# Performance work log

Hardware: AMD Instinct MI355X
Metric: run time of the kernel (lower is better)

Reference implementation:

```python
import jax, jax.numpy as jnp
import numpy as np


def setup_inputs() -> dict:
    key = jax.random.key(0)
    ks = jax.random.split(key, 4)
    B, N, D, C = 8, 32768, 128, 64
    H = D // 2
    features = jax.random.normal(ks[0], (B, N, D), dtype=jnp.float32)
    cluster_assignments = jax.random.randint(ks[1], (B, N), 0, C)
    W1 = jax.random.normal(ks[2], (D, H), dtype=jnp.float32) * (1.0 / np.sqrt(D))
    b1 = jnp.zeros((H,), dtype=jnp.float32)
    W2 = jax.random.normal(ks[3], (H, 1), dtype=jnp.float32) * (1.0 / np.sqrt(H))
    b2 = jnp.zeros((1,), dtype=jnp.float32)
    return {"features": features, "cluster_assignments": cluster_assignments,
            "W1": W1, "b1": b1, "W2": W2, "b2": b2, "num_clusters": C}


def reference(features, cluster_assignments, W1, b1, W2, b2, num_clusters):
    # features: [B, N, D]; cluster_assignments: [B, N] ints in [0, num_clusters)
    B, N, D = features.shape
    # importance_net: Linear -> ReLU -> Linear -> Sigmoid
    h = jax.nn.relu(jnp.einsum('bnd,dh->bnh', features, W1) + b1)
    imp = jax.nn.sigmoid(jnp.einsum('bnh,ho->bno', h, W2) + b2)[..., 0]  # [B, N]

    # Fused per-(batch, cluster) softmax-weighted segment sum.
    num_seg = B * num_clusters
    seg = (cluster_assignments + num_clusters * jnp.arange(B)[:, None]).reshape(-1)  # [B*N]
    imp_f = imp.reshape(-1)
    # stable softmax within each segment
    seg_max = jax.ops.segment_max(imp_f, seg, num_segments=num_seg)  # -inf for empty
    e = jnp.exp(imp_f - seg_max[seg])
    denom = jax.ops.segment_sum(e, seg, num_segments=num_seg)
    w = e / denom[seg]  # [B*N]
    out = jax.ops.segment_sum(features.reshape(-1, D) * w[:, None], seg,
                              num_segments=num_seg)  # empty clusters -> zeros
    return out.reshape(B, num_clusters, D)
```

## Files before the change

kernel.cpp:

```cpp
#include <hip/hip_runtime.h>
#include <hip/hip_bf16.h>


#define B_ 8
#define N_ 32768
#define D_ 128
#define C_ 64
#define H_ 64

#define NTHREADS 512
#define NWAVES 8
#define ROWS_PER_BLOCK 512
#define NBLOCKS ((B_ * N_) / ROWS_PER_BLOCK)
#define SLICES (NBLOCKS / B_)
#define NSS 4
#define RST 152
#define W1S 136

typedef float f32x4 __attribute__((ext_vector_type(4)));
typedef short s16x8 __attribute__((ext_vector_type(8)));

__device__ __forceinline__ short bf16rne(float x) {
    unsigned u = __float_as_uint(x);
    u = (u + 0x7FFFu + ((u >> 16) & 1u)) >> 16;
    return (short)u;
}
__device__ __forceinline__ float ubf_lo(unsigned u) {
    return __uint_as_float(u << 16);
}
__device__ __forceinline__ float ubf_hi(unsigned u) {
    return __uint_as_float(u & 0xFFFF0000u);
}

__device__ __forceinline__ s16x8 pk8(float4 a, float4 b) {
    union { s16x8 v; __hip_bfloat162 h[4]; } u;
    u.h[0] = __float22bfloat162_rn(make_float2(a.x, a.y));
    u.h[1] = __float22bfloat162_rn(make_float2(a.z, a.w));
    u.h[2] = __float22bfloat162_rn(make_float2(b.x, b.y));
    u.h[3] = __float22bfloat162_rn(make_float2(b.z, b.w));
    return u.v;
}

template <bool USE_WS>
__global__ __launch_bounds__(NTHREADS, 2)
void ca_fused_kernel(const float* __restrict__ features,
                     const int* __restrict__ ca,
                     const float* __restrict__ b1,
                     const float* __restrict__ W2,
                     const float* __restrict__ b2,
                     const float* __restrict__ W1,
                     float* __restrict__ out_sums,
                     float* __restrict__ denoms,
                     float* __restrict__ pout,
                     float* __restrict__ pden)
{
    __shared__ __align__(16) unsigned short ft[D_ * RST];
    __shared__ __align__(16) unsigned short w1l[H_ * W1S];
    __shared__ __align__(16) unsigned int ceu[128];

    const int tid  = threadIdx.x;
    const int lane = tid & 63;
    const int wave = tid >> 6;
    const int m    = lane & 15;
    const int kb   = lane >> 4;
    const int kbase = kb * 8;
    const int bidx = blockIdx.x;
    const int b    = bidx / SLICES;
    const int row_blk0 = bidx * ROWS_PER_BLOCK;

    for (int i = tid; i < H_ * D_; i += NTHREADS) {
        const int k = i >> 6, h = i & 63;
        w1l[h * W1S + k] = (unsigned short)bf16rne(W1[i]);
    }

    f32x4 w2v[4];
    unsigned b1p[8];
#pragma unroll
    for (int c4 = 0; c4 < 4; ++c4) {
#pragma unroll
        for (int qq = 0; qq < 4; ++qq)
            w2v[c4][qq] = W2[c4 * 16 + kb * 4 + qq];
#pragma unroll
        for (int hh = 0; hh < 2; ++hh) {
            const int i0 = c4 * 16 + kb * 4 + hh * 2;
            b1p[c4 * 2 + hh] =
                ((unsigned)(unsigned short)bf16rne(b1[i0 + 1]) << 16) |
                (unsigned)(unsigned short)bf16rne(b1[i0]);
        }
    }
    const float b2v = b2[0];

    const int CH = wave >> 1;
    const int dh = wave & 1;

    f32x4 accS[4];
    f32x4 accD = (f32x4){0.f, 0.f, 0.f, 0.f};
#pragma unroll
    for (int nt = 0; nt < 4; ++nt) accS[nt] = (f32x4){0.f, 0.f, 0.f, 0.f};

    s16x8 bones;
    {
        const short o = (m == 0) ? (short)0x3F80 : (short)0;
#pragma unroll
        for (int j = 0; j < 8; ++j) bones[j] = o;
    }
    s16x8 bI0, bI1;
#pragma unroll
    for (int j = 0; j < 8; ++j) {
        bI0[j] = (kbase + j == m)      ? (short)0x3F80 : (short)0;
        bI1[j] = (kbase + j == 16 + m) ? (short)0x3F80 : (short)0;
    }

    const float* fbase = features + (long long)(row_blk0 + wave * 16 + m) * D_;
    float4 pf[8];
#pragma unroll
    for (int ks = 0; ks < 4; ++ks) {
        pf[2 * ks]     = *(const float4*)(fbase + ks * 32 + kbase);
        pf[2 * ks + 1] = *(const float4*)(fbase + ks * 32 + kbase + 4);
    }
    int cv = 0;
    if (lane < 16) cv = ca[row_blk0 + wave * 16 + lane];

    __syncthreads();

#pragma unroll
    for (int ss = 0; ss < NSS; ++ss) {
        s16x8 af[4];
#pragma unroll
        for (int ks = 0; ks < 4; ++ks) af[ks] = pk8(pf[2 * ks], pf[2 * ks + 1]);
        const int cvc = cv;

        if (ss + 1 < NSS) {
            const float* fn = fbase + (ss + 1) * 128 * D_;
#pragma unroll
            for (int ks = 0; ks < 4; ++ks) {
                pf[2 * ks]     = *(const float4*)(fn + ks * 32 + kbase);
                pf[2 * ks + 1] = *(const float4*)(fn + ks * 32 + kbase + 4);
            }
            if (lane < 16) cv = ca[row_blk0 + (ss + 1) * 128 + wave * 16 + lane];
        }
        __builtin_amdgcn_sched_barrier(0);

        const int rg0 = wave * 16 + kb * 4;
#pragma unroll
        for (int ks = 0; ks < 4; ++ks) {
            const f32x4 z = (f32x4){0.f, 0.f, 0.f, 0.f};
            const f32x4 t0 = __builtin_amdgcn_mfma_f32_16x16x32_bf16(af[ks], bI0, z, 0, 0, 0);
            const f32x4 t1 = __builtin_amdgcn_mfma_f32_16x16x32_bf16(af[ks], bI1, z, 0, 0, 0);
            union { uint2 u; __hip_bfloat162 h[2]; } p0, p1;
            p0.h[0] = __float22bfloat162_rn(make_float2(t0[0], t0[1]));
            p0.h[1] = __float22bfloat162_rn(make_float2(t0[2], t0[3]));
            p1.h[0] = __float22bfloat162_rn(make_float2(t1[0], t1[1]));
            p1.h[1] = __float22bfloat162_rn(make_float2(t1[2], t1[3]));
            *(uint2*)&ft[(ks * 32 + m) * RST + rg0]      = p0.u;
            *(uint2*)&ft[(ks * 32 + 16 + m) * RST + rg0] = p1.u;
        }

        float tp = 0.f;
#pragma unroll
        for (int c4 = 0; c4 < 4; ++c4) {
            f32x4 hc = (f32x4){0.f, 0.f, 0.f, 0.f};
#pragma unroll
            for (int ks = 0; ks < 4; ++ks) {
                const s16x8 w = *(const s16x8*)&w1l[(c4 * 16 + m) * W1S +
                                                    ks * 32 + kbase];
                hc = __builtin_amdgcn_mfma_f32_16x16x32_bf16(w, af[ks], hc, 0, 0, 0);
            }
            const float b0  = ubf_lo(b1p[c4 * 2]),     bb1 = ubf_hi(b1p[c4 * 2]);
            const float b2_ = ubf_lo(b1p[c4 * 2 + 1]), b3  = ubf_hi(b1p[c4 * 2 + 1]);
            tp = fmaf(fmaxf(hc[0] + b0,  0.f), w2v[c4][0], tp);
            tp = fmaf(fmaxf(hc[1] + bb1, 0.f), w2v[c4][1], tp);
            tp = fmaf(fmaxf(hc[2] + b2_, 0.f), w2v[c4][2], tp);
            tp = fmaf(fmaxf(hc[3] + b3,  0.f), w2v[c4][3], tp);
        }
        tp += __shfl_xor(tp, 16, 64);
        tp += __shfl_xor(tp, 32, 64);
        const float pre = tp + b2v;
        const float imp = 1.f / (1.f + __expf(-pre));
        const float e   = __expf(imp - 1.f);
        if (lane < 16)
            ceu[wave * 16 + lane] =
                ((unsigned)(unsigned short)bf16rne(e) << 16) | (unsigned)cvc;

        asm volatile("s_waitcnt lgkmcnt(0)" ::: "memory");
        __builtin_amdgcn_s_barrier();

#pragma unroll
        for (int kg = 0; kg < 4; ++kg) {
            const uint4* cq = (const uint4*)&ceu[kg * 32 + kbase];
            const uint4 ua = cq[0], ub = cq[1];
            const unsigned uu[8] = {ua.x, ua.y, ua.z, ua.w, ub.x, ub.y, ub.z, ub.w};

            s16x8 afr;
#pragma unroll
            for (int j = 0; j < 8; ++j)
                afr[j] = ((int)(uu[j] & 0xFFu) == CH * 16 + m)
                             ? (short)(uu[j] >> 16) : (short)0;

#pragma unroll
            for (int nt = 0; nt < 4; ++nt) {
                const int d0 = (dh * 4 + nt) * 16 + m;
                const s16x8 bfv = *(const s16x8*)&ft[d0 * RST + kg * 32 + kbase];
                accS[nt] = __builtin_amdgcn_mfma_f32_16x16x32_bf16(
                    afr, bfv, accS[nt], 0, 0, 0);
            }
            if (dh == 0)
                accD = __builtin_amdgcn_mfma_f32_16x16x32_bf16(afr, bones, accD, 0, 0, 0);
        }

        __builtin_amdgcn_s_barrier();
    }

#pragma unroll
    for (int nt = 0; nt < 4; ++nt)
#pragma unroll
        for (int qq = 0; qq < 4; ++qq) {
            const int idx = (CH * 16 + kb * 4 + qq) * D_ + (dh * 4 + nt) * 16 + m;
            if (USE_WS) pout[(size_t)bidx * (C_ * D_) + idx] = accS[nt][qq];
            else atomicAdd(&out_sums[b * (C_ * D_) + idx], accS[nt][qq]);
        }
    if (dh == 0 && m == 0) {
#pragma unroll
        for (int qq = 0; qq < 4; ++qq) {
            const int c = CH * 16 + kb * 4 + qq;
            if (USE_WS) pden[bidx * C_ + c] = accD[qq];
            else atomicAdd(&denoms[b * C_ + c], accD[qq]);
        }
    }
}

__global__ __launch_bounds__(512)
void ca_reduce_kernel(const float* __restrict__ pout,
                      const float* __restrict__ pden,
                      float* __restrict__ out)
{
    __shared__ float red[512];
    __shared__ float dns;

    const int bc = blockIdx.x;
    const int b  = bc >> 6;
    const int c  = bc & (C_ - 1);
    const int t  = threadIdx.x;
    const int d  = t & 127;
    const int sg = t >> 7;

    const float* pb = pout + ((size_t)(b * SLICES + sg * 16)) * (C_ * D_)
                           + c * D_ + d;
    float s = 0.f;
#pragma unroll 4
    for (int i = 0; i < 16; ++i) s += pb[(size_t)i * (C_ * D_)];
    red[t] = s;

    float dnv = 0.f;
    if (t < SLICES) dnv = pden[(b * SLICES + t) * C_ + c];
    if (t < 64) {
#pragma unroll
        for (int off = 32; off > 0; off >>= 1) dnv += __shfl_xor(dnv, off, 64);
        if (t == 0) dns = dnv;
    }
    __syncthreads();

    if (t < 128) {
        const float tot = red[t] + red[t + 128] + red[t + 256] + red[t + 384];
        const float dn = dns;
        out[(size_t)bc * D_ + t] = (dn > 0.f) ? (tot / dn) : 0.f;
    }
}

__global__ void ca_zero_kernel(float* __restrict__ out_sums,
                               float* __restrict__ denoms)
{
    const int i = blockIdx.x * blockDim.x + threadIdx.x;
    if (i < B_ * C_ * D_) out_sums[i] = 0.f;
    if (i < B_ * C_)      denoms[i] = 0.f;
}

__global__ void ca_finalize_kernel(float* __restrict__ out_sums,
                                   const float* __restrict__ denoms)
{
    const int i = blockIdx.x * blockDim.x + threadIdx.x;
    if (i >= B_ * C_ * D_) return;
    const int bc = i >> 7;
    const float den = denoms[bc];
    const float v = out_sums[i];
    out_sums[i] = (den > 0.f) ? (v / den) : 0.f;
}

extern "C" void kernel_launch(void* const* d_in, const int* in_sizes, int n_in,
                              void* d_out, int out_size, void* d_ws, size_t ws_size,
                              hipStream_t stream) {
    const float* features = (const float*)d_in[0];
    const int*   ca       = (const int*)  d_in[1];
    const float* W1       = (const float*)d_in[2];
    const float* b1       = (const float*)d_in[3];
    const float* W2       = (const float*)d_in[4];
    const float* b2       = (const float*)d_in[5];

    float* out = (float*)d_out;

    float* pden = (float*)d_ws;
    float* pout = (float*)((char*)d_ws + 131072);
    const size_t need_full = 131072 + (size_t)NBLOCKS * C_ * D_ * 4;

    if (ws_size >= need_full) {
        ca_fused_kernel<true><<<NBLOCKS, NTHREADS, 0, stream>>>(
            features, ca, b1, W2, b2, W1, nullptr, nullptr, pout, pden);
        ca_reduce_kernel<<<B_ * C_, 512, 0, stream>>>(pout, pden, out);
    } else {
        ca_zero_kernel<<<(B_ * C_ * D_ + 255) / 256, 256, 0, stream>>>(out, pden);
        ca_fused_kernel<false><<<NBLOCKS, NTHREADS, 0, stream>>>(
            features, ca, b1, W2, b2, W1, out, pden, nullptr, nullptr);
        ca_finalize_kernel<<<(B_ * C_ * D_ + 255) / 256, 256, 0, stream>>>(out, pden);
    }
}
```

Measured before the change: 45.02 us.

## Fuse cross-slice reduction into main kernel via per-batch atomic barrier

Removes the separate reduce kernel. Each block bumps a per-batch atomic counter and spins until all 64 slices of its batch have written their partial sums. It then reduces one (batch, cluster) row of the output. The aim is to drop a dependent kernel launch and let reduction for early-finished batches overlap with other batches. In exchange it adds a memset launch for the counters and a spin-wait that assumes all blocks of a batch are co-resident. It also adds a little extra LDS per block.

```diff
diff --git a/kernel.cpp b/kernel.cpp
--- a/kernel.cpp
+++ b/kernel.cpp
@@ -52,11 +52,15 @@
                      float* __restrict__ out_sums,
                      float* __restrict__ denoms,
                      float* __restrict__ pout,
-                     float* __restrict__ pden)
+                     float* __restrict__ pden,
+                     unsigned* __restrict__ cnt,
+                     float* __restrict__ out)
 {
     __shared__ __align__(16) unsigned short ft[D_ * RST];
     __shared__ __align__(16) unsigned short w1l[H_ * W1S];
     __shared__ __align__(16) unsigned int ceu[128];
+    __shared__ float red[NTHREADS];
+    __shared__ float dns;
 
     const int tid  = threadIdx.x;
     const int lane = tid & 63;
@@ -227,43 +231,48 @@
             else atomicAdd(&denoms[b * C_ + c], accD[qq]);
         }
     }
-}
-
-__global__ __launch_bounds__(512)
-void ca_reduce_kernel(const float* __restrict__ pout,
-                      const float* __restrict__ pden,
-                      float* __restrict__ out)
-{
-    __shared__ float red[512];
-    __shared__ float dns;
-
-    const int bc = blockIdx.x;
-    const int b  = bc >> 6;
-    const int c  = bc & (C_ - 1);
-    const int t  = threadIdx.x;
-    const int d  = t & 127;
-    const int sg = t >> 7;
-
-    const float* pb = pout + ((size_t)(b * SLICES + sg * 16)) * (C_ * D_)
-                           + c * D_ + d;
-    float s = 0.f;
+
+    if (!USE_WS) return;
+
+    __syncthreads();
+    if (tid == 0) {
+        __threadfence();
+        atomicAdd(&cnt[b], 1u);
+        while (__hip_atomic_load(&cnt[b], __ATOMIC_ACQUIRE,
+                                 __HIP_MEMORY_SCOPE_AGENT) < (unsigned)SLICES)
+            __builtin_amdgcn_s_sleep(2);
+    }
+    __syncthreads();
+
+    {
+        const int c  = bidx & (C_ - 1);
+        const int bb = b;
+        const int d  = tid & 127;
+        const int sg = tid >> 7;
+
+        const float* pb = pout + ((size_t)(bb * SLICES + sg * 16)) * (C_ * D_)
+                               + c * D_ + d;
+        float s = 0.f;
 #pragma unroll 4
-    for (int i = 0; i < 16; ++i) s += pb[(size_t)i * (C_ * D_)];
-    red[t] = s;
-
-    float dnv = 0.f;
-    if (t < SLICES) dnv = pden[(b * SLICES + t) * C_ + c];
-    if (t < 64) {
-#pragma unroll
-        for (int off = 32; off > 0; off >>= 1) dnv += __shfl_xor(dnv, off, 64);
-        if (t == 0) dns = dnv;
-    }
-    __syncthreads();
-
-    if (t < 128) {
-        const float tot = red[t] + red[t + 128] + red[t + 256] + red[t + 384];
-        const float dn = dns;
-        out[(size_t)bc * D_ + t] = (dn > 0.f) ? (tot / dn) : 0.f;
+        for (int i = 0; i < 16; ++i) s += pb[(size_t)i * (C_ * D_)];
+        red[tid] = s;
+
+        float dnv = 0.f;
+        if (tid < SLICES) dnv = pden[(bb * SLICES + tid) * C_ + c];
+        if (tid < 64) {
+#pragma unroll
+            for (int off = 32; off > 0; off >>= 1)
+                dnv += __shfl_xor(dnv, off, 64);
+            if (tid == 0) dns = dnv;
+        }
+        __syncthreads();
+
+        if (tid < 128) {
+            const float tot = red[tid] + red[tid + 128] +
+                              red[tid + 256] + red[tid + 384];
+            const float dn = dns;
+            out[(size_t)bidx * D_ + tid] = (dn > 0.f) ? (tot / dn) : 0.f;
+        }
     }
 }
 
@@ -300,16 +309,19 @@
 
     float* pden = (float*)d_ws;
     float* pout = (float*)((char*)d_ws + 131072);
-    const size_t need_full = 131072 + (size_t)NBLOCKS * C_ * D_ * 4;
+    unsigned* cnt = (unsigned*)((char*)d_ws + 131072 +
+                                (size_t)NBLOCKS * C_ * D_ * 4);
+    const size_t need_full = 131072 + (size_t)NBLOCKS * C_ * D_ * 4 + B_ * 4;
 
     if (ws_size >= need_full) {
+        hipMemsetAsync(cnt, 0, B_ * sizeof(unsigned), stream);
         ca_fused_kernel<true><<<NBLOCKS, NTHREADS, 0, stream>>>(
-            features, ca, b1, W2, b2, W1, nullptr, nullptr, pout, pden);
-        ca_reduce_kernel<<<B_ * C_, 512, 0, stream>>>(pout, pden, out);
+            features, ca, b1, W2, b2, W1, nullptr, nullptr, pout, pden, cnt, out);
     } else {
         ca_zero_kernel<<<(B_ * C_ * D_ + 255) / 256, 256, 0, stream>>>(out, pden);
         ca_fused_kernel<false><<<NBLOCKS, NTHREADS, 0, stream>>>(
-            features, ca, b1, W2, b2, W1, out, pden, nullptr, nullptr);
+            features, ca, b1, W2, b2, W1, out, pden, nullptr, nullptr, nullptr,
+            nullptr);
         ca_finalize_kernel<<<(B_ * C_ * D_ + 255) / 256, 256, 0, stream>>>(out, pden);
     }
 }
```

Measured after the change: 105.4 us. +134.1%, slower.
